# Kernel tuning notes

Hardware: AMD Instinct MI355X
Metric: run time of the kernel (lower is better)

Reference implementation:

```python
import jax, jax.numpy as jnp
import numpy as np

N = 50000
E = 800000
D = 128          # node_dim
ED = 64          # edge_dim
H = 4            # n_heads
HD = D // H      # head_dim
LN_EPS = 1e-5


def setup_inputs() -> dict:
    key = jax.random.key(0)
    ks = jax.random.split(key, 10)
    s = 0.05
    return {
        "x": jax.random.normal(ks[0], (N, D), dtype=jnp.float32),
        "edge_index": jax.random.randint(ks[1], (2, E), 0, N, dtype=jnp.int32),
        "edge_attr": jax.random.normal(ks[2], (E, ED), dtype=jnp.float32),
        # parameters (torch Linear transposed to [in, out])
        "align_w": jax.random.normal(ks[3], (2 * D + ED, H), dtype=jnp.float32) * s,
        "align_b": jnp.zeros((H,), dtype=jnp.float32),
        "value_w": jax.random.normal(ks[4], (D, D), dtype=jnp.float32) * s,
        "value_b": jnp.zeros((D,), dtype=jnp.float32),
        "proj_w": jax.random.normal(ks[5], (D, D), dtype=jnp.float32) * s,
        "proj_b": jnp.zeros((D,), dtype=jnp.float32),
        "ln_g": jnp.ones((D,), dtype=jnp.float32),
        "ln_b": jnp.zeros((D,), dtype=jnp.float32),
    }


def reference(x, edge_index, edge_attr, align_w, align_b, value_w, value_b,
              proj_w, proj_b, ln_g, ln_b):
    row, col = edge_index[0], edge_index[1]          # [E], [E]
    h_i = x[row]                                     # [E, D] gather (dst)
    h_j = x[col]                                     # [E, D] gather (src)
    cat_feat = jnp.concatenate([h_i, h_j, edge_attr], axis=-1)  # [E, 2D+ED]
    scores = cat_feat @ align_w + align_b            # [E, H]

    # numerically-stable segment softmax over incoming edges of each dst node
    max_per_node = jax.ops.segment_max(scores, row, num_segments=N)  # [N, H]
    scores_exp = jnp.exp(scores - max_per_node[row])                 # [E, H]
    sum_exp = jax.ops.segment_sum(scores_exp, row, num_segments=N)   # [N, H]
    alpha = scores_exp / (sum_exp[row] + 1e-8)                       # [E, H]

    V = (h_j @ value_w + value_b).reshape(E, H, HD)                  # [E, H, HD]
    weighted = (V * alpha[:, :, None]).reshape(E, D)                 # [E, D]
    context = jax.ops.segment_sum(weighted, row, num_segments=N)     # [N, D]

    y = x + context @ proj_w + proj_b                                # [N, D]
    mu = jnp.mean(y, axis=-1, keepdims=True)
    var = jnp.mean((y - mu) ** 2, axis=-1, keepdims=True)
    return (y - mu) / jnp.sqrt(var + LN_EPS) * ln_g + ln_b
```

## Files before the change

### kernel.cpp

```cpp
#include <hip/hip_runtime.h>
#include <hip/hip_bf16.h>
#include <math.h>

#define N_NODES 50000
#define N_EDGES 800000
#define DIM 128
#define EDIM 64
#define NH 4
#define DEG_CAP 64
#define ESC_BLOCKS 12500
#define BKT_BLOCKS 3125
#define PRE_BLOCKS 1563

__global__ __launch_bounds__(256) void k_prep(
    const int* __restrict__ ei, int* cnt, int2* __restrict__ ecolid,
    const float* __restrict__ x, const float* __restrict__ vw,
    const float* __restrict__ vb, const float* __restrict__ aw,
    const float* __restrict__ ea, float* __restrict__ sexp,
    unsigned int* __restrict__ Vxb, float* __restrict__ aexp) {
    __shared__ float xs[32][129];
    int t = threadIdx.x;
    if (blockIdx.x < ESC_BLOCKS) {
        int l = t & 15, g = t >> 4;
        float wreg[16];
        #pragma unroll
        for (int j = 0; j < 4; ++j)
            #pragma unroll
            for (int h = 0; h < NH; ++h)
                wreg[j * 4 + h] = aw[1024 + (l * 4 + j) * 4 + h];
        int e0 = blockIdx.x * 16 + g;
        #pragma unroll
        for (int k = 0; k < 4; ++k) {
            int e = e0 + k * (ESC_BLOCKS * 16);
            float4 v = *(const float4*)(ea + (size_t)e * EDIM + l * 4);
            float p0 = v.x*wreg[0] + v.y*wreg[4] + v.z*wreg[8]  + v.w*wreg[12];
            float p1 = v.x*wreg[1] + v.y*wreg[5] + v.z*wreg[9]  + v.w*wreg[13];
            float p2 = v.x*wreg[2] + v.y*wreg[6] + v.z*wreg[10] + v.w*wreg[14];
            float p3 = v.x*wreg[3] + v.y*wreg[7] + v.z*wreg[11] + v.w*wreg[15];
            #pragma unroll
            for (int off = 1; off < 4; off <<= 1) {
                p0 += __shfl_xor(p0, off);
                p1 += __shfl_xor(p1, off);
                p2 += __shfl_xor(p2, off);
                p3 += __shfl_xor(p3, off);
            }
            int r = l & 3;
            float pr = (r == 0) ? p0 : (r == 1) ? p1 : (r == 2) ? p2 : p3;
            pr += __shfl_xor(pr, 4);
            pr += __shfl_xor(pr, 8);
            if (l < 4) sexp[(size_t)e * 4 + l] = __expf(pr);
        }
        return;
    }
    if (blockIdx.x < ESC_BLOCKS + BKT_BLOCKS) {
        int e = (blockIdx.x - ESC_BLOCKS) * 256 + t;
        if (e < N_EDGES) {
            int row = ei[e], col = ei[N_EDGES + e];
            int pos = atomicAdd(&cnt[row], 1);
            if (pos < DEG_CAP) ecolid[(size_t)row * DEG_CAP + pos] = make_int2(col, e);
        }
        return;
    }
    int nb = (blockIdx.x - ESC_BLOCKS - BKT_BLOCKS) * 32;
    #pragma unroll
    for (int i = 0; i < 4; ++i) {
        int idx = i * 256 + t;
        int m = idx >> 5, k4 = idx & 31;
        int n = nb + m;
        float4 v = make_float4(0.f, 0.f, 0.f, 0.f);
        if (n < N_NODES) v = *(const float4*)(x + (size_t)n * DIM + k4 * 4);
        xs[m][k4*4+0] = v.x; xs[m][k4*4+1] = v.y; xs[m][k4*4+2] = v.z; xs[m][k4*4+3] = v.w;
    }
    __syncthreads();
    int c = t & 31, mg = t >> 5;
    int d0 = c * 4, m0 = mg * 4;
    float acc[4][4];
    #pragma unroll
    for (int j = 0; j < 4; ++j) { acc[j][0]=0.f; acc[j][1]=0.f; acc[j][2]=0.f; acc[j][3]=0.f; }
    for (int k = 0; k < DIM; ++k) {
        float4 w = *(const float4*)(vw + (size_t)k * DIM + d0);
        #pragma unroll
        for (int j = 0; j < 4; ++j) {
            float xv = xs[m0 + j][k];
            acc[j][0] += xv * w.x; acc[j][1] += xv * w.y;
            acc[j][2] += xv * w.z; acc[j][3] += xv * w.w;
        }
    }
    float4 vb4 = *(const float4*)(vb + d0);
    #pragma unroll
    for (int j = 0; j < 4; ++j) {
        int n = nb + m0 + j;
        if (n < N_NODES) {
            __hip_bfloat162 p0 = __float22bfloat162_rn(
                make_float2(acc[j][0]+vb4.x, acc[j][1]+vb4.y));
            __hip_bfloat162 p1 = __float22bfloat162_rn(
                make_float2(acc[j][2]+vb4.z, acc[j][3]+vb4.w));
            uint2 u;
            u.x = *reinterpret_cast<unsigned int*>(&p0);
            u.y = *reinterpret_cast<unsigned int*>(&p1);
            *(uint2*)(Vxb + (size_t)n * 64 + c * 2) = u;
        }
    }
    if (t < 128) {
        int m = t >> 2, h = t & 3;
        float s = 0.f;
        for (int k = 0; k < DIM; ++k) s += xs[m][k] * aw[(size_t)(DIM + k) * NH + h];
        int n = nb + m;
        if (n < N_NODES) aexp[(size_t)n * NH + h] = __expf(s);
    }
}

__global__ __launch_bounds__(256) void k_mega(
    const int* __restrict__ cnt, const int2* __restrict__ ecolid,
    const float* __restrict__ sexp, const float* __restrict__ aexp,
    const unsigned int* __restrict__ Vxb, float* __restrict__ context) {
    int t = threadIdx.x;
    int lane = t & 63, w = t >> 6;
    int n = blockIdx.x * 4 + w;
    if (n >= N_NODES) return;
    int l = lane & 15, grp = lane >> 4;
    int hd = l >> 2;
    int deg = cnt[n]; deg = deg < DEG_CAP ? deg : DEG_CAP;
    int2 ce = (lane < deg) ? ecolid[(size_t)n * DEG_CAP + lane] : make_int2(0, 0);
    int colv = ce.x, eidv = ce.y;
    float a0=0.f,a1=0.f,a2=0.f,a3=0.f,a4=0.f,a5=0.f,a6=0.f,a7=0.f,sw=0.f;
    int jm4 = (deg + 3) & ~3;
    #pragma unroll 4
    for (int j = grp; j < jm4; j += 4) {
        int col = __shfl(colv, j);
        int eid = __shfl(eidv, j);
        float wgt = 0.f;
        if (j < deg)
            wgt = sexp[(size_t)eid * 4 + hd] * aexp[(size_t)col * NH + hd];
        uint4 u = *(const uint4*)(Vxb + (size_t)col * 64 + l * 4);
        float f0 = __uint_as_float(u.x << 16), f1 = __uint_as_float(u.x & 0xffff0000u);
        float f2 = __uint_as_float(u.y << 16), f3 = __uint_as_float(u.y & 0xffff0000u);
        float f4 = __uint_as_float(u.z << 16), f5 = __uint_as_float(u.z & 0xffff0000u);
        float f6 = __uint_as_float(u.w << 16), f7 = __uint_as_float(u.w & 0xffff0000u);
        a0 += f0*wgt; a1 += f1*wgt; a2 += f2*wgt; a3 += f3*wgt;
        a4 += f4*wgt; a5 += f5*wgt; a6 += f6*wgt; a7 += f7*wgt;
        sw += wgt;
    }
    #pragma unroll
    for (int off = 16; off < 64; off <<= 1) {
        a0 += __shfl_xor(a0, off); a1 += __shfl_xor(a1, off);
        a2 += __shfl_xor(a2, off); a3 += __shfl_xor(a3, off);
        a4 += __shfl_xor(a4, off); a5 += __shfl_xor(a5, off);
        a6 += __shfl_xor(a6, off); a7 += __shfl_xor(a7, off);
        sw += __shfl_xor(sw, off);
    }
    if (lane < 16) {
        float inv = 1.0f / (sw + 1e-8f);
        float* cp = context + (size_t)n * DIM + l * 8;
        *(float4*)(cp)     = make_float4(a0*inv, a1*inv, a2*inv, a3*inv);
        *(float4*)(cp + 4) = make_float4(a4*inv, a5*inv, a6*inv, a7*inv);
    }
}

__global__ __launch_bounds__(128) void k_proj_ln(
    const float* __restrict__ x, const float* __restrict__ context,
    const float* __restrict__ pw, const float* __restrict__ pb,
    const float* __restrict__ lg, const float* __restrict__ lb,
    float* __restrict__ out) {
    __shared__ float cs[32][129];
    int t = threadIdx.x;
    int nb = blockIdx.x * 32;
    #pragma unroll
    for (int i = 0; i < 8; ++i) {
        int idx = i * 128 + t;
        int m = idx >> 5, k4 = idx & 31;
        int n = nb + m;
        float4 v = make_float4(0.f, 0.f, 0.f, 0.f);
        if (n < N_NODES) v = *(const float4*)(context + (size_t)n * DIM + k4 * 4);
        cs[m][k4*4+0] = v.x; cs[m][k4*4+1] = v.y; cs[m][k4*4+2] = v.z; cs[m][k4*4+3] = v.w;
    }
    __syncthreads();
    int c = t & 31, mg = t >> 5;
    int d0 = c * 4, m0 = mg * 8;
    float acc[8][4];
    #pragma unroll
    for (int j = 0; j < 8; ++j) { acc[j][0]=0.f; acc[j][1]=0.f; acc[j][2]=0.f; acc[j][3]=0.f; }
    for (int k = 0; k < DIM; ++k) {
        float4 w = *(const float4*)(pw + (size_t)k * DIM + d0);
        #pragma unroll
        for (int j = 0; j < 8; ++j) {
            float cv = cs[m0 + j][k];
            acc[j][0] += cv * w.x; acc[j][1] += cv * w.y;
            acc[j][2] += cv * w.z; acc[j][3] += cv * w.w;
        }
    }
    float4 pb4 = *(const float4*)(pb + d0);
    float4 g4  = *(const float4*)(lg + d0);
    float4 b4  = *(const float4*)(lb + d0);
    #pragma unroll
    for (int j = 0; j < 8; ++j) {
        int n = nb + m0 + j;
        float4 xv = make_float4(0.f, 0.f, 0.f, 0.f);
        if (n < N_NODES) xv = *(const float4*)(x + (size_t)n * DIM + d0);
        float y0 = xv.x + acc[j][0] + pb4.x;
        float y1 = xv.y + acc[j][1] + pb4.y;
        float y2 = xv.z + acc[j][2] + pb4.z;
        float y3 = xv.w + acc[j][3] + pb4.w;
        float ps = y0 + y1 + y2 + y3;
        float pq = y0*y0 + y1*y1 + y2*y2 + y3*y3;
        #pragma unroll
        for (int off = 1; off < 32; off <<= 1) {
            ps += __shfl_xor(ps, off);
            pq += __shfl_xor(pq, off);
        }
        float mu = ps * (1.0f / DIM);
        float var = pq * (1.0f / DIM) - mu * mu;
        float rstd = rsqrtf(var + 1e-5f);
        if (n < N_NODES) {
            float4 o;
            o.x = (y0 - mu) * rstd * g4.x + b4.x;
            o.y = (y1 - mu) * rstd * g4.y + b4.y;
            o.z = (y2 - mu) * rstd * g4.z + b4.z;
            o.w = (y3 - mu) * rstd * g4.w + b4.w;
            *(float4*)(out + (size_t)n * DIM + d0) = o;
        }
    }
}

extern "C" void kernel_launch(void* const* d_in, const int* in_sizes, int n_in,
                              void* d_out, int out_size, void* d_ws, size_t ws_size,
                              hipStream_t stream) {
    const float* x       = (const float*)d_in[0];
    const int*   ei      = (const int*)  d_in[1];
    const float* ea      = (const float*)d_in[2];
    const float* align_w = (const float*)d_in[3];
    const float* value_w = (const float*)d_in[5];
    const float* value_b = (const float*)d_in[6];
    const float* proj_w  = (const float*)d_in[7];
    const float* proj_b  = (const float*)d_in[8];
    const float* ln_g    = (const float*)d_in[9];
    const float* ln_b    = (const float*)d_in[10];
    float* out = (float*)d_out;
    float* ws  = (float*)d_ws;

    unsigned int* Vxb = (unsigned int*)ws;
    float* aexp    = ws + 3200000;
    float* sexp    = ws + 3400000;
    float* context = ws + 6600000;
    int2*  ecolid  = (int2*)(ws + 13000000);
    int*   cnt     = (int*)(ws + 19400000);

    hipMemsetAsync(cnt, 0, (size_t)N_NODES * sizeof(int), stream);
    k_prep<<<ESC_BLOCKS + BKT_BLOCKS + PRE_BLOCKS, 256, 0, stream>>>(
        ei, cnt, ecolid, x, value_w, value_b, align_w, ea, sexp, Vxb, aexp);
    k_mega<<<N_NODES / 4, 256, 0, stream>>>(
        cnt, ecolid, sexp, aexp, Vxb, context);
    k_proj_ln<<<(N_NODES + 31) / 32, 128, 0, stream>>>(
        x, context, proj_w, proj_b, ln_g, ln_b, out);
}
```

Measured before the change: 228.0 us.

## Merge edge-score and bucketing blocks into one thread-per-edge branch

The edge-attribute score computation (16 lanes per edge with shuffle reductions) and the edge bucketing pass are folded into a single branch where each thread handles one edge. That thread computes the four head scores with align weights staged in shared memory, writes exp scores as one float4, and then does the atomic bucket insert. This cuts block count and shuffle overhead. The cost is that each thread reads a 256-byte row, so loads across a wavefront are strided rather than coalesced.

```diff
diff --git a/kernel.cpp b/kernel.cpp
--- a/kernel.cpp
+++ b/kernel.cpp
@@ -8,8 +8,7 @@
 #define EDIM 64
 #define NH 4
 #define DEG_CAP 64
-#define ESC_BLOCKS 12500
-#define BKT_BLOCKS 3125
+#define EDG_BLOCKS 3125
 #define PRE_BLOCKS 1563
 
 __global__ __launch_bounds__(256) void k_prep(
@@ -19,49 +18,34 @@
     const float* __restrict__ ea, float* __restrict__ sexp,
     unsigned int* __restrict__ Vxb, float* __restrict__ aexp) {
     __shared__ float xs[32][129];
+    __shared__ float s_w[256];
     int t = threadIdx.x;
-    if (blockIdx.x < ESC_BLOCKS) {
-        int l = t & 15, g = t >> 4;
-        float wreg[16];
-        #pragma unroll
-        for (int j = 0; j < 4; ++j)
-            #pragma unroll
-            for (int h = 0; h < NH; ++h)
-                wreg[j * 4 + h] = aw[1024 + (l * 4 + j) * 4 + h];
-        int e0 = blockIdx.x * 16 + g;
-        #pragma unroll
-        for (int k = 0; k < 4; ++k) {
-            int e = e0 + k * (ESC_BLOCKS * 16);
-            float4 v = *(const float4*)(ea + (size_t)e * EDIM + l * 4);
-            float p0 = v.x*wreg[0] + v.y*wreg[4] + v.z*wreg[8]  + v.w*wreg[12];
-            float p1 = v.x*wreg[1] + v.y*wreg[5] + v.z*wreg[9]  + v.w*wreg[13];
-            float p2 = v.x*wreg[2] + v.y*wreg[6] + v.z*wreg[10] + v.w*wreg[14];
-            float p3 = v.x*wreg[3] + v.y*wreg[7] + v.z*wreg[11] + v.w*wreg[15];
-            #pragma unroll
-            for (int off = 1; off < 4; off <<= 1) {
-                p0 += __shfl_xor(p0, off);
-                p1 += __shfl_xor(p1, off);
-                p2 += __shfl_xor(p2, off);
-                p3 += __shfl_xor(p3, off);
-            }
-            int r = l & 3;
-            float pr = (r == 0) ? p0 : (r == 1) ? p1 : (r == 2) ? p2 : p3;
-            pr += __shfl_xor(pr, 4);
-            pr += __shfl_xor(pr, 8);
-            if (l < 4) sexp[(size_t)e * 4 + l] = __expf(pr);
-        }
+    if (blockIdx.x < EDG_BLOCKS) {
+        s_w[t] = aw[1024 + t];
+        __syncthreads();
+        int e = blockIdx.x * 256 + t;
+        const float4* ep = (const float4*)(ea + (size_t)e * EDIM);
+        float h0 = 0.f, h1 = 0.f, h2 = 0.f, h3 = 0.f;
+        #pragma unroll
+        for (int i = 0; i < 16; ++i) {
+            float4 v = ep[i];
+            float4 w0 = *(const float4*)&s_w[(i * 4 + 0) * 4];
+            float4 w1 = *(const float4*)&s_w[(i * 4 + 1) * 4];
+            float4 w2 = *(const float4*)&s_w[(i * 4 + 2) * 4];
+            float4 w3 = *(const float4*)&s_w[(i * 4 + 3) * 4];
+            h0 += v.x*w0.x + v.y*w1.x + v.z*w2.x + v.w*w3.x;
+            h1 += v.x*w0.y + v.y*w1.y + v.z*w2.y + v.w*w3.y;
+            h2 += v.x*w0.z + v.y*w1.z + v.z*w2.z + v.w*w3.z;
+            h3 += v.x*w0.w + v.y*w1.w + v.z*w2.w + v.w*w3.w;
+        }
+        float4 se = make_float4(__expf(h0), __expf(h1), __expf(h2), __expf(h3));
+        *(float4*)(sexp + (size_t)e * 4) = se;
+        int row = ei[e], col = ei[N_EDGES + e];
+        int pos = atomicAdd(&cnt[row], 1);
+        if (pos < DEG_CAP) ecolid[(size_t)row * DEG_CAP + pos] = make_int2(col, e);
         return;
     }
-    if (blockIdx.x < ESC_BLOCKS + BKT_BLOCKS) {
-        int e = (blockIdx.x - ESC_BLOCKS) * 256 + t;
-        if (e < N_EDGES) {
-            int row = ei[e], col = ei[N_EDGES + e];
-            int pos = atomicAdd(&cnt[row], 1);
-            if (pos < DEG_CAP) ecolid[(size_t)row * DEG_CAP + pos] = make_int2(col, e);
-        }
-        return;
-    }
-    int nb = (blockIdx.x - ESC_BLOCKS - BKT_BLOCKS) * 32;
+    int nb = (blockIdx.x - EDG_BLOCKS) * 32;
     #pragma unroll
     for (int i = 0; i < 4; ++i) {
         int idx = i * 256 + t;
@@ -246,7 +230,7 @@
     int*   cnt     = (int*)(ws + 19400000);
 
     hipMemsetAsync(cnt, 0, (size_t)N_NODES * sizeof(int), stream);
-    k_prep<<<ESC_BLOCKS + BKT_BLOCKS + PRE_BLOCKS, 256, 0, stream>>>(
+    k_prep<<<EDG_BLOCKS + PRE_BLOCKS, 256, 0, stream>>>(
         ei, cnt, ecolid, x, value_w, value_b, align_w, ea, sexp, Vxb, aexp);
     k_mega<<<N_NODES / 4, 256, 0, stream>>>(
         cnt, ecolid, sexp, aexp, Vxb, context);
```

Result: faster. 219.4 us (-3.8%).
